# Performance work log

Measured on AMD Instinct MI355X. Metric: run time of the kernel, lower is better.

## Reference

```python
import jax, jax.numpy as jnp
import numpy as np

B, S, D, H, F = 2, 2048, 1024, 16, 4096
DH = D // H
EPS = 1e-6


def layer_norm(x, g, b):
    mu = jnp.mean(x, axis=-1, keepdims=True)
    var = jnp.mean(jnp.square(x - mu), axis=-1, keepdims=True)
    return (x - mu) * jax.lax.rsqrt(var + EPS) * g + b


def setup_inputs() -> dict:
    key = jax.random.key(0)
    ks = jax.random.split(key, 12)
    s_in = 1.0 / np.sqrt(D)
    s_ff = 1.0 / np.sqrt(F)
    return {
        "x_enc": jax.random.normal(ks[0], (B, S, D), jnp.float32),
        "x_pos": jax.random.normal(ks[1], (B, S, D), jnp.float32),
        "wq": jax.random.normal(ks[2], (D, D), jnp.float32) * s_in,
        "bq": jnp.zeros((D,), jnp.float32),
        "wk": jax.random.normal(ks[3], (D, D), jnp.float32) * s_in,
        "bk": jnp.zeros((D,), jnp.float32),
        "wv": jax.random.normal(ks[4], (D, D), jnp.float32) * s_in,
        "bv": jnp.zeros((D,), jnp.float32),
        "wc": jax.random.normal(ks[5], (D, D), jnp.float32) * s_in,
        "bc": jnp.zeros((D,), jnp.float32),
        "w1": jax.random.normal(ks[6], (D, F), jnp.float32) * s_in,
        "b1": jnp.zeros((F,), jnp.float32),
        "w2": jax.random.normal(ks[7], (F, D), jnp.float32) * s_ff,
        "b2": jnp.zeros((D,), jnp.float32),
        "g1": jnp.ones((D,), jnp.float32),
        "be1": jnp.zeros((D,), jnp.float32),
        "g2": jnp.ones((D,), jnp.float32),
        "be2": jnp.zeros((D,), jnp.float32),
    }


def reference(x_enc, x_pos, wq, bq, wk, bk, wv, bv, wc, bc, w1, b1, w2, b2, g1, be1, g2, be2):
    x = x_enc + x_pos  # [B,S,D]

    def split_heads(t):  # [B,S,D] -> [B,H,S,DH]
        return t.reshape(B, S, H, DH).transpose(0, 2, 1, 3)

    q = split_heads(x @ wq + bq)
    k = split_heads(x @ wk + bk)
    v = split_heads(x @ wv + bv)

    scale = jax.lax.rsqrt(jnp.asarray(DH, jnp.float32))
    logits = jnp.einsum("bhqd,bhkd->bhqk", q, k) * scale  # [B,H,S,S]
    weights = jax.nn.softmax(logits, axis=-1)
    attn = jnp.einsum("bhqk,bhkd->bhqd", weights, v)  # [B,H,S,DH]
    attn = attn.transpose(0, 2, 1, 3).reshape(B, S, D)
    attn = attn @ wc + bc

    # residual: x + LN(attn_out)   (dropout inactive in eval)
    a = x + layer_norm(attn, g1, be1)
    ffn = jnp.maximum(a @ w1 + b1, 0.0) @ w2 + b2
    out = a + layer_norm(ffn, g2, be2)
    return out
```

## Files before the change

kernel.cpp:

```cpp
#include <hip/hip_runtime.h>
#include <math.h>

#define B_ 2
#define S_ 2048
#define D_ 1024
#define H_ 16
#define F_ 4096

typedef __bf16 bf16_t;
typedef __bf16 bf16x8 __attribute__((ext_vector_type(8)));
typedef __bf16 bf16x4 __attribute__((ext_vector_type(4)));
typedef float f32x4 __attribute__((ext_vector_type(4)));
typedef float f32x16 __attribute__((ext_vector_type(16)));
typedef _Float16 f16x4 __attribute__((ext_vector_type(4)));
typedef _Float16 f16x8 __attribute__((ext_vector_type(8)));
typedef __fp16 h16x2 __attribute__((ext_vector_type(2)));

__device__ __forceinline__ bf16_t f2b(float f) { return (bf16_t)f; }

__device__ __forceinline__ void gld_lds16(const void* g, void* l) {
  __builtin_amdgcn_global_load_lds(
      (const __attribute__((address_space(1))) unsigned int*)g,
      (__attribute__((address_space(3))) unsigned int*)l, 16, 0, 0);
}

__device__ __forceinline__ void transpose_tile(const float* __restrict__ in,
                                               bf16_t* __restrict__ out,
                                               int K, int N, int bx, int by) {
  __shared__ float tile[64][65];
  int k0 = by * 64, n0 = bx * 64;
  int tid = threadIdx.x;
  int col4 = tid & 15;
  int row = tid >> 4;
#pragma unroll
  for (int rr = 0; rr < 4; ++rr) {
    int r = rr * 16 + row;
    float4 v = *reinterpret_cast<const float4*>(in + (size_t)(k0 + r) * N + n0 + col4 * 4);
    tile[r][col4 * 4 + 0] = v.x;
    tile[r][col4 * 4 + 1] = v.y;
    tile[r][col4 * 4 + 2] = v.z;
    tile[r][col4 * 4 + 3] = v.w;
  }
  __syncthreads();
#pragma unroll
  for (int rr = 0; rr < 4; ++rr) {
    int n = rr * 16 + row;
    bf16x4 o;
    o[0] = f2b(tile[col4 * 4 + 0][n]);
    o[1] = f2b(tile[col4 * 4 + 1][n]);
    o[2] = f2b(tile[col4 * 4 + 2][n]);
    o[3] = f2b(tile[col4 * 4 + 3][n]);
    *reinterpret_cast<bf16x4*>(out + (size_t)(n0 + n) * K + k0 + col4 * 4) = o;
  }
}

__global__ __launch_bounds__(256) void prep_kernel(
    const float* __restrict__ xe, const float* __restrict__ xp,
    bf16_t* __restrict__ XB,
    const float* __restrict__ wq, const float* __restrict__ wk,
    const float* __restrict__ wv, const float* __restrict__ wc,
    const float* __restrict__ w1, const float* __restrict__ w2,
    const float* __restrict__ bq, const float* __restrict__ bk,
    const float* __restrict__ bv,
    bf16_t* __restrict__ Wqkvt, bf16_t* __restrict__ wctb,
    bf16_t* __restrict__ w1tb, bf16_t* __restrict__ w2tb,
    float* __restrict__ bqkv) {
  int bid = blockIdx.x;
  if (bid < 4096) {
    int i = bid * 256 + threadIdx.x;
    float4 av = reinterpret_cast<const float4*>(xe)[i];
    float4 bv4 = reinterpret_cast<const float4*>(xp)[i];
    bf16x4 o;
    o[0] = f2b(av.x + bv4.x); o[1] = f2b(av.y + bv4.y);
    o[2] = f2b(av.z + bv4.z); o[3] = f2b(av.w + bv4.w);
    reinterpret_cast<bf16x4*>(XB)[i] = o;
    return;
  }
  int pb = bid - 4096;
  if (pb < 1024) {
    int seg = pb >> 8, local = pb & 255;
    const float* src = seg == 0 ? wq : (seg == 1 ? wk : (seg == 2 ? wv : wc));
    bf16_t* dst = seg == 3 ? wctb : Wqkvt + (size_t)seg * D_ * D_;
    transpose_tile(src, dst, D_, D_, local & 15, local >> 4);
  } else if (pb < 2048) {
    int local = pb - 1024;
    transpose_tile(w1, w1tb, D_, F_, local & 63, local >> 6);
  } else if (pb < 3072) {
    int local = pb - 2048;
    transpose_tile(w2, w2tb, F_, D_, local & 15, local >> 4);
  } else {
    int i = (pb - 3072) * 256 + threadIdx.x;
    const float* src = i < 1024 ? bq : (i < 2048 ? bk : bv);
    bqkv[i] = src[i & 1023];
  }
}


__device__ __forceinline__ void stage_half(const bf16_t* __restrict__ G,
                                           int grow0, int K, int kt,
                                           bf16_t* lb, int tid) {
#pragma unroll
  for (int c = 0; c < 2; ++c) {
    int e = c * 512 + tid;
    int rl = e >> 3, kg = e & 7;
    int kgs = kg ^ (rl & 7);
    gld_lds16(G + (size_t)(grow0 + rl) * K + kt + kgs * 8, lb + e * 8);
  }
}

template <int DBUF, int MH, int NH, int SARR, int SBUF, int SH, int DOWAIT>
__device__ __forceinline__ void gemm_phase(
    bf16_t* As, bf16_t* Bs, const bf16_t* __restrict__ A,
    const bf16_t* __restrict__ Bt, f32x16 (&acc)[4][2], int bm, int bn, int K,
    int kbeg, int stile, int tid, int m32, int khalf, int ra0, int ra1, int rb) {
  const bf16_t* abase = As + (DBUF * 2 + MH) * 8192;
  const bf16_t* bbase = Bs + (DBUF * 2 + NH) * 8192;
  bf16x8 af0[4], af1[4], bfx[4];
#pragma unroll
  for (int kc = 0; kc < 4; ++kc) {
    int kg = ((kc * 2 + khalf) ^ (m32 & 7)) * 8;
    af0[kc] = *reinterpret_cast<const bf16x8*>(abase + ra0 * 64 + kg);
    af1[kc] = *reinterpret_cast<const bf16x8*>(abase + ra1 * 64 + kg);
    bfx[kc] = *reinterpret_cast<const bf16x8*>(bbase + rb * 64 + kg);
  }
  {
    const bf16_t* G = SARR ? Bt : A;
    int g0 = (SARR ? bn : bm) + SH * 128;
    bf16_t* lb = (SARR ? Bs : As) + (SBUF * 2 + SH) * 8192;
    stage_half(G, g0, K, kbeg + stile * 64, lb, tid);
  }
  if (DOWAIT) asm volatile("s_waitcnt vmcnt(4)" ::: "memory");
  __builtin_amdgcn_s_barrier();
  asm volatile("s_waitcnt lgkmcnt(0)" ::: "memory");
  __builtin_amdgcn_sched_barrier(0);
  __builtin_amdgcn_s_setprio(1);
#pragma unroll
  for (int kc = 0; kc < 4; ++kc) {
    acc[MH * 2 + 0][NH] = __builtin_amdgcn_mfma_f32_32x32x16_bf16(
        af0[kc], bfx[kc], acc[MH * 2 + 0][NH], 0, 0, 0);
    acc[MH * 2 + 1][NH] = __builtin_amdgcn_mfma_f32_32x32x16_bf16(
        af1[kc], bfx[kc], acc[MH * 2 + 1][NH], 0, 0, 0);
  }
  __builtin_amdgcn_s_setprio(0);
  __builtin_amdgcn_s_barrier();
}

__global__ __launch_bounds__(512) void gemm_kernel(
    const bf16_t* __restrict__ A, const bf16_t* __restrict__ Bt,
    const float* __restrict__ bias,
    bf16_t* __restrict__ P0, bf16_t* __restrict__ P1,
    bf16_t* __restrict__ P2, bf16_t* __restrict__ P3,
    _Float16* __restrict__ VTout,
    int M, int N, int K, int relu, int kchunk, int rx, int ry) {
  __shared__ bf16_t As[4 * 8192];
  __shared__ bf16_t Bs[4 * 8192];
  int tid = threadIdx.x;
  int lane = tid & 63, wave = tid >> 6;
  int bx = blockIdx.x, by = blockIdx.y;
  if (rx) {
    int id = by * gridDim.x + bx;
    int j = id & 7, local = id >> 3;
    int regs_x = gridDim.x / rx;
    bx = (j % regs_x) * rx + local % rx;
    by = (j / regs_x) * ry + local / rx;
  }
  int bm = by * 256, bn = bx * 256;
  int wm = wave >> 2, wn = wave & 3;
  int m32 = lane & 31, khalf = lane >> 5;
  int ra0 = wm * 64 + m32, ra1 = ra0 + 32, rb = wn * 32 + m32;
  int z = blockIdx.z;
  int kbeg = z * kchunk;
  int nt = kchunk >> 6, ntm1 = nt - 1;
  f32x16 acc[4][2] = {};

  stage_half(A, bm, K, kbeg, As + 0 * 8192, tid);
  stage_half(Bt, bn, K, kbeg, Bs + 0 * 8192, tid);
  stage_half(A, bm + 128, K, kbeg, As + 1 * 8192, tid);
  stage_half(Bt, bn + 128, K, kbeg, Bs + 1 * 8192, tid);
  stage_half(A, bm, K, kbeg + 64, As + 2 * 8192, tid);
  stage_half(Bt, bn, K, kbeg + 64, Bs + 2 * 8192, tid);
  asm volatile("s_waitcnt vmcnt(4)" ::: "memory");
  __builtin_amdgcn_s_barrier();

  int nt2 = nt >> 1;
  for (int j = 0; j < nt2; ++j) {
    int t1 = 2 * j + 1;
    int t2 = 2 * j + 2 > ntm1 ? ntm1 : 2 * j + 2;
    int t3 = 2 * j + 3 > ntm1 ? ntm1 : 2 * j + 3;
    gemm_phase<0, 0, 0, 0, 1, 1, 0>(As, Bs, A, Bt, acc, bm, bn, K, kbeg, t1, tid, m32, khalf, ra0, ra1, rb);
    gemm_phase<0, 0, 1, 1, 1, 1, 0>(As, Bs, A, Bt, acc, bm, bn, K, kbeg, t1, tid, m32, khalf, ra0, ra1, rb);
    gemm_phase<0, 1, 0, 0, 0, 0, 0>(As, Bs, A, Bt, acc, bm, bn, K, kbeg, t2, tid, m32, khalf, ra0, ra1, rb);
    gemm_phase<0, 1, 1, 1, 0, 0, 1>(As, Bs, A, Bt, acc, bm, bn, K, kbeg, t2, tid, m32, khalf, ra0, ra1, rb);
    gemm_phase<1, 0, 0, 0, 0, 1, 0>(As, Bs, A, Bt, acc, bm, bn, K, kbeg, t2, tid, m32, khalf, ra0, ra1, rb);
    gemm_phase<1, 0, 1, 1, 0, 1, 0>(As, Bs, A, Bt, acc, bm, bn, K, kbeg, t2, tid, m32, khalf, ra0, ra1, rb);
    gemm_phase<1, 1, 0, 0, 1, 0, 0>(As, Bs, A, Bt, acc, bm, bn, K, kbeg, t3, tid, m32, khalf, ra0, ra1, rb);
    gemm_phase<1, 1, 1, 1, 1, 0, 1>(As, Bs, A, Bt, acc, bm, bn, K, kbeg, t3, tid, m32, khalf, ra0, ra1, rb);
  }

  bf16_t* Cb = z == 0 ? P0 : (z == 1 ? P1 : (z == 2 ? P2 : P3));
#pragma unroll
  for (int ni = 0; ni < 2; ++ni) {
    int n = bn + ni * 128 + wn * 32 + m32;
    float bz = (bias && z == 0) ? bias[n] : 0.f;
#pragma unroll
    for (int mi = 0; mi < 4; ++mi) {
      float vv[16];
#pragma unroll
      for (int r = 0; r < 16; ++r) {
        float v = acc[mi][ni][r] + bz;
        if (relu) v = fmaxf(v, 0.f);
        vv[r] = v;
      }
      int sb = bm + (mi >> 1) * 128 + wm * 64 + (mi & 1) * 32;
      if (VTout && n >= 2048) {
        int h = (n - 2048) >> 6, d = (n - 2048) & 63;
        int bb = sb >> 11;
        _Float16* vtr = VTout + ((size_t)((bb * H_ + h) * 64 + d)) * S_ + (sb & 2047);
#pragma unroll
        for (int g = 0; g < 4; ++g) {
          int off = ((2 * g + khalf) & 3) * 8 + (g >> 1) * 4;
          f16x4 hv;
          hv[0] = (_Float16)vv[g * 4 + 0]; hv[1] = (_Float16)vv[g * 4 + 1];
          hv[2] = (_Float16)vv[g * 4 + 2]; hv[3] = (_Float16)vv[g * 4 + 3];
          *reinterpret_cast<f16x4*>(vtr + off) = hv;
        }
      } else {
#pragma unroll
        for (int r = 0; r < 16; ++r) {
          int m = sb + (r & 3) + 8 * (r >> 2) + 4 * khalf;
          Cb[(size_t)m * N + n] = f2b(vv[r]);
        }
      }
    }
  }
}

__global__ __launch_bounds__(256) void attn_kernel(const bf16_t* __restrict__ Q,
                                                   const bf16_t* __restrict__ Kg,
                                                   const _Float16* __restrict__ VT,
                                                   bf16_t* __restrict__ O, int ldq) {
  __shared__ bf16_t Ks[128 * 64];
  __shared__ _Float16 Vs[64 * 128];
  int qt = blockIdx.x, h = blockIdx.y, b = blockIdx.z;
  int tid = threadIdx.x, wave = tid >> 6, lane = tid & 63;
  int qcol = lane & 15, grp = lane >> 4;
  int qbase = qt * 64 + wave * 16;
  const float kS = 0.125f * 1.4426950408889634f;
  const float kB = 12.0f * 1.4426950408889634f;
  const h16x2 one2 = {(__fp16)1.f, (__fp16)1.f};

  bf16x8 qf[2];
#pragma unroll
  for (int c = 0; c < 2; ++c)
    qf[c] = *reinterpret_cast<const bf16x8*>(
        Q + (size_t)(b * S_ + qbase + qcol) * ldq + h * 64 + c * 32 + grp * 8);
  const _Float16* vtb = VT + (size_t)((b * H_ + h) * 64) * S_;

  f32x4 oacc[4] = {};
  float lsum = 0.f;

  for (int t0 = 0; t0 < S_; t0 += 128) {
    __syncthreads();
#pragma unroll
    for (int cc = 0; cc < 4; ++cc) {
      int e = cc * 256 + tid;
      int row = e >> 3, kg = e & 7, kgs = kg ^ (row & 7);
      gld_lds16(Kg + (size_t)(b * S_ + t0 + row) * ldq + h * 64 + kgs * 8, Ks + e * 8);
    }
#pragma unroll
    for (int cc = 0; cc < 4; ++cc) {
      int e = cc * 256 + tid;
      int d = e >> 4, kc = e & 15, kcs = kc ^ (d & 7);
      gld_lds16(vtb + (size_t)d * S_ + t0 + kcs * 8, Vs + e * 8);
    }
    __syncthreads();
#pragma unroll
    for (int kb2 = 0; kb2 < 4; ++kb2) {
      f32x4 se = {}, so = {};
      int krowe = kb2 * 32 + qcol;
      int krowo = krowe + 16;
#pragma unroll
      for (int c = 0; c < 2; ++c) {
        int gce = (c * 4 + grp) ^ (krowe & 7);
        bf16x8 kfe = *reinterpret_cast<const bf16x8*>(Ks + krowe * 64 + gce * 8);
        se = __builtin_amdgcn_mfma_f32_16x16x32_bf16(kfe, qf[c], se, 0, 0, 0);
        int gco = (c * 4 + grp) ^ (krowo & 7);
        bf16x8 kfo = *reinterpret_cast<const bf16x8*>(Ks + krowo * 64 + gco * 8);
        so = __builtin_amdgcn_mfma_f32_16x16x32_bf16(kfo, qf[c], so, 0, 0, 0);
      }
      float pe0 = __builtin_amdgcn_exp2f(fmaf(se[0], kS, -kB));
      float pe1 = __builtin_amdgcn_exp2f(fmaf(se[1], kS, -kB));
      float pe2 = __builtin_amdgcn_exp2f(fmaf(se[2], kS, -kB));
      float pe3 = __builtin_amdgcn_exp2f(fmaf(se[3], kS, -kB));
      float po0 = __builtin_amdgcn_exp2f(fmaf(so[0], kS, -kB));
      float po1 = __builtin_amdgcn_exp2f(fmaf(so[1], kS, -kB));
      float po2 = __builtin_amdgcn_exp2f(fmaf(so[2], kS, -kB));
      float po3 = __builtin_amdgcn_exp2f(fmaf(so[3], kS, -kB));
      h16x2 e01 = __builtin_amdgcn_cvt_pkrtz(pe0, pe1);
      h16x2 e23 = __builtin_amdgcn_cvt_pkrtz(pe2, pe3);
      h16x2 q01 = __builtin_amdgcn_cvt_pkrtz(po0, po1);
      h16x2 q23 = __builtin_amdgcn_cvt_pkrtz(po2, po3);
      lsum = __builtin_amdgcn_fdot2(e01, one2, lsum, false);
      lsum = __builtin_amdgcn_fdot2(e23, one2, lsum, false);
      lsum = __builtin_amdgcn_fdot2(q01, one2, lsum, false);
      lsum = __builtin_amdgcn_fdot2(q23, one2, lsum, false);
      f16x8 pf;
      pf[0] = (_Float16)e01[0]; pf[1] = (_Float16)e01[1];
      pf[2] = (_Float16)e23[0]; pf[3] = (_Float16)e23[1];
      pf[4] = (_Float16)q01[0]; pf[5] = (_Float16)q01[1];
      pf[6] = (_Float16)q23[0]; pf[7] = (_Float16)q23[1];
#pragma unroll
      for (int db = 0; db < 4; ++db) {
        int d = db * 16 + qcol;
        int kc = (kb2 * 4 + grp) ^ (d & 7);
        f16x8 vf = *reinterpret_cast<const f16x8*>(Vs + d * 128 + kc * 8);
        oacc[db] = __builtin_amdgcn_mfma_f32_16x16x32_f16(vf, pf, oacc[db], 0, 0, 0);
      }
    }
  }

  lsum += __shfl_xor(lsum, 16, 64);
  lsum += __shfl_xor(lsum, 32, 64);
  float inv = 1.f / lsum;
  size_t rowbase = (size_t)(b * S_ + qbase + qcol) * D_ + h * 64;
#pragma unroll
  for (int db = 0; db < 4; ++db)
#pragma unroll
    for (int r = 0; r < 4; ++r)
      O[rowbase + db * 16 + grp * 4 + r] = f2b(oacc[db][r] * inv);
}

__global__ __launch_bounds__(256) void ln_res_kernel(const bf16_t* Y0,
                                                     const bf16_t* Y1,
                                                     const bf16_t* Y2,
                                                     const bf16_t* Y3,
                                                     int nY,
                                                     const bf16_t* Xres,
                                                     const float* __restrict__ g,
                                                     const float* __restrict__ be,
                                                     float* OutF,
                                                     bf16_t* OutB) {
  int row = blockIdx.x;
  int tid = threadIdx.x, wave = tid >> 6, lane = tid & 63;
  size_t base = (size_t)row * D_;
  bf16x4 y0 = reinterpret_cast<const bf16x4*>(Y0 + base)[tid];
  bf16x4 y1 = reinterpret_cast<const bf16x4*>(Y1 + base)[tid];
  float4 v;
  v.x = (float)y0[0] + (float)y1[0];
  v.y = (float)y0[1] + (float)y1[1];
  v.z = (float)y0[2] + (float)y1[2];
  v.w = (float)y0[3] + (float)y1[3];
  if (nY == 4) {
    bf16x4 y2 = reinterpret_cast<const bf16x4*>(Y2 + base)[tid];
    bf16x4 y3 = reinterpret_cast<const bf16x4*>(Y3 + base)[tid];
    v.x += (float)y2[0] + (float)y3[0];
    v.y += (float)y2[1] + (float)y3[1];
    v.z += (float)y2[2] + (float)y3[2];
    v.w += (float)y2[3] + (float)y3[3];
  }
  float s = v.x + v.y + v.z + v.w;
  float s2 = v.x * v.x + v.y * v.y + v.z * v.z + v.w * v.w;
#pragma unroll
  for (int off = 32; off > 0; off >>= 1) {
    s += __shfl_xor(s, off, 64);
    s2 += __shfl_xor(s2, off, 64);
  }
  __shared__ float red[2][4];
  if (lane == 0) { red[0][wave] = s; red[1][wave] = s2; }
  __syncthreads();
  s = red[0][0] + red[0][1] + red[0][2] + red[0][3];
  s2 = red[1][0] + red[1][1] + red[1][2] + red[1][3];
  float mu = s * (1.f / D_);
  float var = s2 * (1.f / D_) - mu * mu;
  float rstd = rsqrtf(var + 1e-6f);
  bf16x4 xr4 = reinterpret_cast<const bf16x4*>(Xres + base)[tid];
  float4 gv = reinterpret_cast<const float4*>(g)[tid];
  float4 bv = reinterpret_cast<const float4*>(be)[tid];
  float4 o;
  o.x = (float)xr4[0] + (v.x - mu) * rstd * gv.x + bv.x;
  o.y = (float)xr4[1] + (v.y - mu) * rstd * gv.y + bv.y;
  o.z = (float)xr4[2] + (v.z - mu) * rstd * gv.z + bv.z;
  o.w = (float)xr4[3] + (v.w - mu) * rstd * gv.w + bv.w;
  if (OutF) reinterpret_cast<float4*>(OutF + base)[tid] = o;
  if (OutB) {
    bf16x4 ob; ob[0] = f2b(o.x); ob[1] = f2b(o.y); ob[2] = f2b(o.z); ob[3] = f2b(o.w);
    reinterpret_cast<bf16x4*>(OutB + base)[tid] = ob;
  }
}

extern "C" void kernel_launch(void* const* d_in, const int* in_sizes, int n_in,
                              void* d_out, int out_size, void* d_ws, size_t ws_size,
                              hipStream_t stream) {
  const float* x_enc = (const float*)d_in[0];
  const float* x_pos = (const float*)d_in[1];
  const float* wq = (const float*)d_in[2];
  const float* bq = (const float*)d_in[3];
  const float* wk = (const float*)d_in[4];
  const float* bk = (const float*)d_in[5];
  const float* wv = (const float*)d_in[6];
  const float* bv = (const float*)d_in[7];
  const float* wc = (const float*)d_in[8];
  const float* bc = (const float*)d_in[9];
  const float* w1 = (const float*)d_in[10];
  const float* b1 = (const float*)d_in[11];
  const float* w2 = (const float*)d_in[12];
  const float* b2 = (const float*)d_in[13];
  const float* g1 = (const float*)d_in[14];
  const float* be1 = (const float*)d_in[15];
  const float* g2 = (const float*)d_in[16];
  const float* be2 = (const float*)d_in[17];

  const size_t MB = 1024ull * 1024ull;
  char* w = (char*)d_ws;
  bf16_t* F0 = (bf16_t*)(w + 0);
  bf16_t* F1p = (bf16_t*)(w + 8 * MB);
  bf16_t* Wqkvt = (bf16_t*)(w + 32 * MB);
  bf16_t* wctb = (bf16_t*)(w + 38 * MB);
  bf16_t* w1tb = (bf16_t*)(w + 40 * MB);
  bf16_t* w2tb = (bf16_t*)(w + 48 * MB);
  bf16_t* XB = (bf16_t*)(w + 56 * MB);
  bf16_t* QKVB = (bf16_t*)(w + 64 * MB);
  bf16_t* Pp0 = (bf16_t*)(w + 64 * MB);
  bf16_t* Pp1 = (bf16_t*)(w + 72 * MB);
  bf16_t* Pp2 = (bf16_t*)(w + 80 * MB);
  bf16_t* F2 = (bf16_t*)(w + 64 * MB);
  bf16_t* F3 = (bf16_t*)(w + 72 * MB);
  bf16_t* ATTNB = (bf16_t*)(w + 88 * MB);
  float* bqkv = (float*)(w + 96 * MB);
  _Float16* VTg = (_Float16*)(w + 104 * MB);
  bf16_t* Pp3 = (bf16_t*)(w + 104 * MB);
  bf16_t* F1B = (bf16_t*)(w + 112 * MB);

  const int rows = B_ * S_;

  prep_kernel<<<7180, 256, 0, stream>>>(x_enc, x_pos, XB,
                                        wq, wk, wv, wc, w1, w2, bq, bk, bv,
                                        Wqkvt, wctb, w1tb, w2tb, bqkv);

  gemm_kernel<<<dim3(3 * D_ / 256, rows / 256, 1), 512, 0, stream>>>(
      XB, Wqkvt, bqkv, QKVB, nullptr, nullptr, nullptr, VTg,
      rows, 3 * D_, D_, 0, D_, 3, 8);

  attn_kernel<<<dim3(S_ / 64, H_, B_), 256, 0, stream>>>(
      QKVB, QKVB + D_, VTg, ATTNB, 3 * D_);

  gemm_kernel<<<dim3(D_ / 256, rows / 256, 4), 512, 0, stream>>>(
      ATTNB, wctb, bc, Pp0, Pp1, Pp2, Pp3, nullptr,
      rows, D_, D_, 0, D_ / 4, 2, 4);

  ln_res_kernel<<<rows, 256, 0, stream>>>(Pp0, Pp1, Pp2, Pp3, 4, XB, g1, be1,
                                          nullptr, XB);

  gemm_kernel<<<dim3(F_ / 256, rows / 256, 1), 512, 0, stream>>>(
      XB, w1tb, b1, F1B, nullptr, nullptr, nullptr, nullptr,
      rows, F_, D_, 1, D_, 4, 8);

  gemm_kernel<<<dim3(D_ / 256, rows / 256, 4), 512, 0, stream>>>(
      F1B, w2tb, b2, F0, F1p, F2, F3, nullptr,
      rows, D_, F_, 0, F_ / 4, 2, 4);

  ln_res_kernel<<<rows, 256, 0, stream>>>(F0, F1p, F2, F3, 4, XB, g2, be2,
                                          (float*)d_out, nullptr);
}
```

Before: 374.5 us.

## Double-buffer K/V tiles in attention and double block to 128 queries

The attention kernel now keeps two LDS buffers for K and V and prefetches the next 128-key tile while the current one is consumed, using a single barrier per iteration. The block grows to 512 threads covering 128 queries, which halves K/V tile loads per query. s_setprio is raised around the PV MFMAs. In exchange, LDS use per block doubles, the grid halves to 512 blocks, and occupancy may drop.

Result: no change. 376.3 us (+0.5%).

```diff
diff --git a/kernel.cpp b/kernel.cpp
--- a/kernel.cpp
+++ b/kernel.cpp
@@ -235,16 +235,16 @@
   }
 }
 
-__global__ __launch_bounds__(256) void attn_kernel(const bf16_t* __restrict__ Q,
+__global__ __launch_bounds__(512) void attn_kernel(const bf16_t* __restrict__ Q,
                                                    const bf16_t* __restrict__ Kg,
                                                    const _Float16* __restrict__ VT,
                                                    bf16_t* __restrict__ O, int ldq) {
-  __shared__ bf16_t Ks[128 * 64];
-  __shared__ _Float16 Vs[64 * 128];
+  __shared__ bf16_t Ks[2][128 * 64];
+  __shared__ _Float16 Vs[2][64 * 128];
   int qt = blockIdx.x, h = blockIdx.y, b = blockIdx.z;
   int tid = threadIdx.x, wave = tid >> 6, lane = tid & 63;
   int qcol = lane & 15, grp = lane >> 4;
-  int qbase = qt * 64 + wave * 16;
+  int qbase = qt * 128 + wave * 16;
   const float kS = 0.125f * 1.4426950408889634f;
   const float kB = 12.0f * 1.4426950408889634f;
   const h16x2 one2 = {(__fp16)1.f, (__fp16)1.f};
@@ -259,21 +259,31 @@
   f32x4 oacc[4] = {};
   float lsum = 0.f;
 
+#define ATTN_STAGE(BUF, T0)                                                     \
+  {                                                                             \
+    _Pragma("unroll") for (int cc = 0; cc < 2; ++cc) {                          \
+      int e = cc * 512 + tid;                                                   \
+      int row = e >> 3, kg = e & 7, kgs = kg ^ (row & 7);                       \
+      gld_lds16(Kg + (size_t)(b * S_ + (T0) + row) * ldq + h * 64 + kgs * 8,    \
+                &Ks[BUF][0] + e * 8);                                           \
+    }                                                                           \
+    _Pragma("unroll") for (int cc = 0; cc < 2; ++cc) {                          \
+      int e = cc * 512 + tid;                                                   \
+      int d = e >> 4, kc = e & 15, kcs = kc ^ (d & 7);                          \
+      gld_lds16(vtb + (size_t)d * S_ + (T0) + kcs * 8, &Vs[BUF][0] + e * 8);    \
+    }                                                                           \
+  }
+
+  ATTN_STAGE(0, 0);
+  __syncthreads();
+
+  int buf = 0;
   for (int t0 = 0; t0 < S_; t0 += 128) {
-    __syncthreads();
-#pragma unroll
-    for (int cc = 0; cc < 4; ++cc) {
-      int e = cc * 256 + tid;
-      int row = e >> 3, kg = e & 7, kgs = kg ^ (row & 7);
-      gld_lds16(Kg + (size_t)(b * S_ + t0 + row) * ldq + h * 64 + kgs * 8, Ks + e * 8);
+    if (t0 + 128 < S_) {
+      if (buf == 0) ATTN_STAGE(1, t0 + 128) else ATTN_STAGE(0, t0 + 128);
     }
-#pragma unroll
-    for (int cc = 0; cc < 4; ++cc) {
-      int e = cc * 256 + tid;
-      int d = e >> 4, kc = e & 15, kcs = kc ^ (d & 7);
-      gld_lds16(vtb + (size_t)d * S_ + t0 + kcs * 8, Vs + e * 8);
-    }
-    __syncthreads();
+    const bf16_t* ksb = &Ks[buf][0];
+    const _Float16* vsb = &Vs[buf][0];
 #pragma unroll
     for (int kb2 = 0; kb2 < 4; ++kb2) {
       f32x4 se = {}, so = {};
@@ -282,10 +292,10 @@
 #pragma unroll
       for (int c = 0; c < 2; ++c) {
         int gce = (c * 4 + grp) ^ (krowe & 7);
-        bf16x8 kfe = *reinterpret_cast<const bf16x8*>(Ks + krowe * 64 + gce * 8);
+        bf16x8 kfe = *reinterpret_cast<const bf16x8*>(ksb + krowe * 64 + gce * 8);
         se = __builtin_amdgcn_mfma_f32_16x16x32_bf16(kfe, qf[c], se, 0, 0, 0);
         int gco = (c * 4 + grp) ^ (krowo & 7);
-        bf16x8 kfo = *reinterpret_cast<const bf16x8*>(Ks + krowo * 64 + gco * 8);
+        bf16x8 kfo = *reinterpret_cast<const bf16x8*>(ksb + krowo * 64 + gco * 8);
         so = __builtin_amdgcn_mfma_f32_16x16x32_bf16(kfo, qf[c], so, 0, 0, 0);
       }
       float pe0 = __builtin_amdgcn_exp2f(fmaf(se[0], kS, -kB));
@@ -309,15 +319,20 @@
       pf[2] = (_Float16)e23[0]; pf[3] = (_Float16)e23[1];
       pf[4] = (_Float16)q01[0]; pf[5] = (_Float16)q01[1];
       pf[6] = (_Float16)q23[0]; pf[7] = (_Float16)q23[1];
+      __builtin_amdgcn_s_setprio(1);
 #pragma unroll
       for (int db = 0; db < 4; ++db) {
         int d = db * 16 + qcol;
         int kc = (kb2 * 4 + grp) ^ (d & 7);
-        f16x8 vf = *reinterpret_cast<const f16x8*>(Vs + d * 128 + kc * 8);
+        f16x8 vf = *reinterpret_cast<const f16x8*>(vsb + d * 128 + kc * 8);
         oacc[db] = __builtin_amdgcn_mfma_f32_16x16x32_f16(vf, pf, oacc[db], 0, 0, 0);
       }
+      __builtin_amdgcn_s_setprio(0);
     }
-  }
+    __syncthreads();
+    buf ^= 1;
+  }
+#undef ATTN_STAGE
 
   lsum += __shfl_xor(lsum, 16, 64);
   lsum += __shfl_xor(lsum, 32, 64);
@@ -441,7 +456,7 @@
       XB, Wqkvt, bqkv, QKVB, nullptr, nullptr, nullptr, VTg,
       rows, 3 * D_, D_, 0, D_, 3, 8);
 
-  attn_kernel<<<dim3(S_ / 64, H_, B_), 256, 0, stream>>>(
+  attn_kernel<<<dim3(S_ / 128, H_, B_), 512, 0, stream>>>(
       QKVB, QKVB + D_, VTg, ATTNB, 3 * D_);
 
   gemm_kernel<<<dim3(D_ / 256, rows / 256, 4), 512, 0, stream>>>(
```
